# Kernel optimization log

Measured on AMD Instinct MI355X. Metric: run time of the kernel, lower is better.

## Reference

```python
import jax, jax.numpy as jnp
import numpy as np

T, H, E, F, K, FS = 2048, 2048, 64, 512, 8, 512


def setup_inputs() -> dict:
    key = jax.random.key(0)
    ks = jax.random.split(key, 6)
    s = 0.02
    return {
        "hidden_states": jax.random.normal(ks[0], (T, H), jnp.float32),
        # merged gate: E router logits + 1 shared-expert gate logit
        "W_gate": jax.random.normal(ks[1], (H, E + 1), jnp.float32) * s,
        # per-expert merged gate_up proj: [E, H, 2F]
        "W_gate_up": jax.random.normal(ks[2], (E, H, 2 * F), jnp.float32) * s,
        "W_down": jax.random.normal(ks[3], (E, F, H), jnp.float32) * s,
        # shared expert
        "Ws_gate_up": jax.random.normal(ks[4], (H, 2 * FS), jnp.float32) * s,
        "Ws_down": jax.random.normal(ks[5], (FS, H), jnp.float32) * s,
    }


def reference(hidden_states, W_gate, W_gate_up, W_down, Ws_gate_up, Ws_down):
    x = hidden_states  # [T, H]
    logits_all = x @ W_gate                      # [T, E+1]
    router_logits = logits_all[:, :E]
    shared_gate_logit = logits_all[:, E:]        # [T, 1]

    # FusedMoE routing: softmax -> top_k -> renormalize (norm_topk_prob=True)
    probs = jax.nn.softmax(router_logits.astype(jnp.float32), axis=-1)
    topk_w, topk_idx = jax.lax.top_k(probs, K)   # [T, K]
    topk_w = topk_w / jnp.sum(topk_w, axis=-1, keepdims=True)
    # dense combine weights [T, E] (zero for unselected experts)
    combine = jnp.zeros((T, E), probs.dtype).at[
        jnp.arange(T)[:, None], topk_idx].set(topk_w)

    # grouped expert GEMMs (dense reference: every expert sees all tokens,
    # combine-weights zero-out unrouted pairs)
    gu = jnp.einsum('th,ehf->etf', x, W_gate_up)   # [E, T, 2F]
    g, u = jnp.split(gu, 2, axis=-1)
    act = jax.nn.silu(g) * u                       # [E, T, F]
    # apply combine weight before down-proj to avoid [E, T, H] intermediate
    act = act * combine.T[:, :, None].astype(act.dtype)
    routed = jnp.einsum('etf,efh->th', act, W_down)  # [T, H]

    # shared expert (Qwen3NextMLP with sigmoid expert_gate)
    sgu = x @ Ws_gate_up                           # [T, 2FS]
    sg, su = jnp.split(sgu, 2, axis=-1)
    shared = (jax.nn.silu(sg) * su) @ Ws_down      # [T, H]
    shared = jax.nn.sigmoid(shared_gate_logit) * shared

    return shared + routed.astype(x.dtype)
```

## Files before the change

### kernel.cpp

```cpp
#include <hip/hip_runtime.h>
#include <hip/hip_bf16.h>
#include <math.h>

#define T_TOK 2048
#define H_DIM 2048
#define E_NUM 64
#define F_DIM 512
#define K_TOP 8
#define FS_DIM 512
#define NROWS (T_TOK * K_TOP)

typedef __attribute__((ext_vector_type(8))) short short8v;
typedef __attribute__((ext_vector_type(4))) float f32x4;

static __device__ __forceinline__ unsigned short f2bf(float f) {
    unsigned int u = __float_as_uint(f);
    u += 0x7fff + ((u >> 16) & 1);
    return (unsigned short)(u >> 16);
}

#define ASWZ(row) (((row) + ((row) >> 3)) & 7)

typedef const unsigned int __attribute__((address_space(1))) gu32;
typedef unsigned int __attribute__((address_space(3))) lu32;
#define GLDS16(gsrc, ldst) \
    __builtin_amdgcn_global_load_lds((gu32*)(gsrc), (lu32*)(ldst), 16, 0, 0)
#define SB0() __builtin_amdgcn_sched_barrier(0)

__global__ __launch_bounds__(256) void cvt_bf16_kernel(
    const float* __restrict__ in, unsigned short* __restrict__ out, int n8)
{
    int i = blockIdx.x * 256 + threadIdx.x;
    if (i < n8) {
        const float4* p = (const float4*)(in + (size_t)i * 8);
        float4 v0 = p[0], v1 = p[1];
        ushort4 a = make_ushort4(f2bf(v0.x), f2bf(v0.y), f2bf(v0.z), f2bf(v0.w));
        ushort4 b = make_ushort4(f2bf(v1.x), f2bf(v1.y), f2bf(v1.z), f2bf(v1.w));
        ushort4* q = (ushort4*)(out + (size_t)i * 8);
        q[0] = a; q[1] = b;
    }
}

__global__ __launch_bounds__(64) void router_kernel(
    const float* __restrict__ x, const float* __restrict__ Wg,
    int* __restrict__ topk_idx, float* __restrict__ topk_w,
    float* __restrict__ sgate, int* __restrict__ counts)
{
    const int t = blockIdx.x;
    const int lane = threadIdx.x;
    const float* xr = x + (size_t)t * H_DIM;

    float a0 = 0.f, a1 = 0.f, a2 = 0.f, a3 = 0.f;
    for (int h = 0; h < H_DIM; h += 4) {
        float4 xv = *(const float4*)&xr[h];
        a0 += xv.x * Wg[(h + 0) * 65 + lane];
        a1 += xv.y * Wg[(h + 1) * 65 + lane];
        a2 += xv.z * Wg[(h + 2) * 65 + lane];
        a3 += xv.w * Wg[(h + 3) * 65 + lane];
    }
    float logit = (a0 + a1) + (a2 + a3);

    float a64 = 0.f;
    for (int h = lane; h < H_DIM; h += 64) a64 += xr[h] * Wg[h * 65 + 64];
#pragma unroll
    for (int off = 32; off >= 1; off >>= 1) a64 += __shfl_xor(a64, off);

    float v = logit;
    float selv[K_TOP]; int seli[K_TOP];
#pragma unroll
    for (int k = 0; k < K_TOP; ++k) {
        float mv = v; int mi = lane;
#pragma unroll
        for (int off = 32; off >= 1; off >>= 1) {
            float ov = __shfl_xor(mv, off);
            int   oi = __shfl_xor(mi, off);
            if (ov > mv || (ov == mv && oi < mi)) { mv = ov; mi = oi; }
        }
        selv[k] = mv; seli[k] = mi;
        if (lane == mi) v = -INFINITY;
    }

    if (lane == 0) {
        float m = selv[0];
        float w[K_TOP]; float s = 0.f;
#pragma unroll
        for (int k = 0; k < K_TOP; ++k) { w[k] = __expf(selv[k] - m); s += w[k]; }
        float inv = 1.f / s;
#pragma unroll
        for (int k = 0; k < K_TOP; ++k) {
            topk_idx[t * K_TOP + k] = seli[k];
            topk_w[t * K_TOP + k] = w[k] * inv;
            atomicAdd(&counts[seli[k]], 1);
        }
        sgate[t] = 1.f / (1.f + __expf(-a64));
    }
}

__global__ __launch_bounds__(256) void bucket_kernel(
    const int* __restrict__ topk_idx, const float* __restrict__ topk_w,
    const int* __restrict__ counts, int* __restrict__ offsets,
    int* __restrict__ bucket_tok, float* __restrict__ bucket_w)
{
    const int e = blockIdx.x, thr = threadIdx.x;
    __shared__ int cnt[256];
    __shared__ int base_s;
    const int q0 = thr * 64;
    int c = 0;
    for (int q = 0; q < 64; ++q) c += (topk_idx[q0 + q] == e) ? 1 : 0;
    cnt[thr] = c;
    __syncthreads();
    if (thr == 0) {
        int off = 0;
        for (int i = 0; i < e; ++i) off += counts[i];
        offsets[e] = off;
        base_s = off;
        int run = 0;
        for (int i = 0; i < 256; ++i) { int tval = cnt[i]; cnt[i] = run; run += tval; }
    }
    __syncthreads();
    int pos = base_s + cnt[thr];
    for (int q = 0; q < 64; ++q) {
        int pp = q0 + q;
        if (topk_idx[pp] == e) {
            bucket_tok[pos] = pp >> 3;
            bucket_w[pos] = topk_w[pp];
            ++pos;
        }
    }
}

__global__ __launch_bounds__(256) void transpose_cvt_kernel(
    const float* __restrict__ in, unsigned short* __restrict__ out,
    int R, int C)
{
    const int e = blockIdx.z;
    in  += (size_t)e * R * C;
    out += (size_t)e * R * C;
    const int c0 = blockIdx.x * 64, r0 = blockIdx.y * 64;
    __shared__ unsigned short tile[64][72];
    const int t = threadIdx.x;
    const int cc = (t & 15) * 4;
#pragma unroll
    for (int i = 0; i < 4; ++i) {
        int r = (t >> 4) + i * 16;
        float4 v = *(const float4*)&in[(size_t)(r0 + r) * C + c0 + cc];
        tile[cc + 0][r] = f2bf(v.x);
        tile[cc + 1][r] = f2bf(v.y);
        tile[cc + 2][r] = f2bf(v.z);
        tile[cc + 3][r] = f2bf(v.w);
    }
    __syncthreads();
    const int c = t >> 2, j = t & 3;
    uint4 v0 = *(const uint4*)&tile[c][j * 16];
    uint4 v1 = *(const uint4*)&tile[c][j * 16 + 8];
    uint4* dst = (uint4*)&out[(size_t)(c0 + c) * R + r0 + j * 16];
    dst[0] = v0; dst[1] = v1;
}

template<bool ROUTED>
__global__ __launch_bounds__(256, 2) void gu_mfma_kernel(
    const unsigned short* __restrict__ xb,
    const unsigned short* __restrict__ WT,
    const int* __restrict__ counts, const int* __restrict__ offsets,
    const int* __restrict__ bucket_tok, const float* __restrict__ bucket_w,
    unsigned short* __restrict__ actout)
{
    constexpr int BM = 128;
    __shared__ __align__(16) unsigned short As[2][BM * 64];
    __shared__ __align__(16) unsigned short Bs[2][128 * 64];
    __shared__ int   toksS[BM];
    __shared__ float twsS[BM];

    const int tid  = threadIdx.x;
    const int lane = tid & 63;
    const int wid  = tid >> 6;
    const int wm = wid >> 1, wn = wid & 1;
    const int lrow = lane & 15, lhi = lane >> 4;

    int cblk, ne, base, e;
    if (ROUTED) {
        int nw = (blockIdx.x & 7) * ((int)gridDim.x >> 3) + (blockIdx.x >> 3);
        e = nw >> 3; cblk = nw & 7;
        ne = counts[e]; base = offsets[e];
    } else {
        e = E_NUM; cblk = blockIdx.x;
        ne = T_TOK; base = 0;
    }
    const int c0 = cblk * 64;
    const unsigned short* We = WT + (size_t)e * (2 * F_DIM) * H_DIM;

    int rdB[4][2];
#pragma unroll
    for (int fn = 0; fn < 4; ++fn) {
        int r = ((fn & 1) ? 16 : 0) + wn * 32 + lrow + ((fn >> 1) ? 64 : 0);
#pragma unroll
        for (int ks = 0; ks < 2; ++ks) {
            int kc = ks * 4 + lhi;
            rdB[fn][ks] = r * 64 + ((kc ^ ASWZ(r)) & 7) * 8;
        }
    }
    int rdA[4][2];
#pragma unroll
    for (int fm = 0; fm < 4; ++fm) {
        int arow = wm * 64 + fm * 16 + lrow;
#pragma unroll
        for (int ks = 0; ks < 2; ++ks) {
            int kc = ks * 4 + lhi;
            rdA[fm][ks] = arow * 64 + ((kc ^ ASWZ(arow)) & 7) * 8;
        }
    }
    int bsrc[4];
#pragma unroll
    for (int i = 0; i < 4; ++i) {
        int n = wid * 32 + i * 8 + (lane >> 3);
        int grow = (n < 64) ? (c0 + n) : (F_DIM + c0 + (n - 64));
        bsrc[i] = grow * H_DIM + (((lane & 7) ^ ASWZ(n)) << 3);
    }
    const int NT = H_DIM / 64;

    const int m0_beg = ROUTED ? 0 : blockIdx.y * BM;
    const int m0_end = ROUTED ? ne : m0_beg + BM;

    for (int m0 = m0_beg; m0 < m0_end; m0 += BM) {
        __syncthreads();
        if (tid < BM) {
            int idx = m0 + tid; bool v = idx < ne;
            if (ROUTED) {
                toksS[tid] = v ? bucket_tok[base + idx] : bucket_tok[base];
                twsS[tid]  = v ? bucket_w[base + idx] : 0.f;
            } else {
                toksS[tid] = v ? idx : (T_TOK - 1);
                twsS[tid]  = 1.f;
            }
        }
        __syncthreads();

        int asrc[4];
#pragma unroll
        for (int i = 0; i < 4; ++i) {
            int row = wid * 32 + i * 8 + (lane >> 3);
            asrc[i] = toksS[row] * H_DIM + (((lane & 7) ^ ASWZ(row)) << 3);
        }

        f32x4 acc[4][4];
#pragma unroll
        for (int i = 0; i < 4; ++i)
#pragma unroll
            for (int j = 0; j < 4; ++j) acc[i][j] = (f32x4){0.f, 0.f, 0.f, 0.f};

#pragma unroll
        for (int i = 0; i < 4; ++i) GLDS16(xb + asrc[i], &As[0][(wid * 32 + i * 8) * 64]);
#pragma unroll
        for (int i = 0; i < 4; ++i) GLDS16(We + bsrc[i], &Bs[0][(wid * 32 + i * 8) * 64]);
#pragma unroll
        for (int i = 0; i < 4; ++i) GLDS16(xb + asrc[i] + 64, &As[1][(wid * 32 + i * 8) * 64]);
#pragma unroll
        for (int i = 0; i < 4; ++i) GLDS16(We + bsrc[i] + 64, &Bs[1][(wid * 32 + i * 8) * 64]);
        SB0();

        for (int kt = 0; kt < NT; ++kt) {
            if (kt + 1 < NT) asm volatile("s_waitcnt vmcnt(8)" ::: "memory");
            else             asm volatile("s_waitcnt vmcnt(0)" ::: "memory");
            SB0();
            __builtin_amdgcn_s_barrier();
            SB0();
            const unsigned short* A_ = As[kt & 1];
            const unsigned short* B_ = Bs[kt & 1];
            __builtin_amdgcn_s_setprio(1);
#pragma unroll
            for (int ks = 0; ks < 2; ++ks) {
                short8v bf[4];
#pragma unroll
                for (int fn = 0; fn < 4; ++fn) bf[fn] = *(const short8v*)&B_[rdB[fn][ks]];
#pragma unroll
                for (int fm = 0; fm < 4; ++fm) {
                    short8v af = *(const short8v*)&A_[rdA[fm][ks]];
#pragma unroll
                    for (int fn = 0; fn < 4; ++fn)
                        acc[fm][fn] = __builtin_amdgcn_mfma_f32_16x16x32_bf16(
                            af, bf[fn], acc[fm][fn], 0, 0, 0);
                }
            }
            __builtin_amdgcn_s_setprio(0);
            SB0();
            __builtin_amdgcn_s_barrier();
            SB0();
            if (kt + 2 < NT) {
                const int kn = (kt + 2) * 64;
#pragma unroll
                for (int i = 0; i < 4; ++i)
                    GLDS16(xb + asrc[i] + kn, &As[kt & 1][(wid * 32 + i * 8) * 64]);
#pragma unroll
                for (int i = 0; i < 4; ++i)
                    GLDS16(We + bsrc[i] + kn, &Bs[kt & 1][(wid * 32 + i * 8) * 64]);
                SB0();
            }
        }

#pragma unroll
        for (int fm = 0; fm < 4; ++fm) {
#pragma unroll
            for (int p = 0; p < 2; ++p) {
                const int acol = c0 + wn * 32 + p * 16 + lrow;
#pragma unroll
                for (int i = 0; i < 4; ++i) {
                    int ml = wm * 64 + fm * 16 + lhi * 4 + i;
                    int idx = m0 + ml;
                    if (idx < ne) {
                        float gv = acc[fm][p][i], uv = acc[fm][p + 2][i];
                        float sg = gv / (1.f + __expf(-gv));
                        float val = sg * uv * twsS[ml];
                        size_t orow = ROUTED ? (size_t)(base + idx) : (size_t)idx;
                        actout[orow * F_DIM + acol] = f2bf(val);
                    }
                }
            }
        }
    }
}

template<bool ROUTED>
__global__ __launch_bounds__(256, 2) void down_mfma_kernel(
    const unsigned short* __restrict__ actb,
    const unsigned short* __restrict__ WT,
    const int* __restrict__ counts, const int* __restrict__ offsets,
    const int* __restrict__ bucket_tok, const float* __restrict__ sgate,
    float* __restrict__ out)
{
    constexpr int BM = 128;
    __shared__ __align__(16) unsigned short As[2][BM * 64];
    __shared__ __align__(16) unsigned short Bs[2][128 * 64];
    __shared__ int   toksS[BM];
    __shared__ float sgS[BM];

    const int tid  = threadIdx.x;
    const int lane = tid & 63;
    const int wid  = tid >> 6;
    const int wm = wid >> 1, wn = wid & 1;
    const int lrow = lane & 15, lhi = lane >> 4;

    int cblk, ne, base, e;
    if (ROUTED) {
        int nw = (blockIdx.x & 7) * ((int)gridDim.x >> 3) + (blockIdx.x >> 3);
        e = nw >> 4; cblk = nw & 15;
        ne = counts[e]; base = offsets[e];
    } else {
        e = E_NUM; cblk = blockIdx.x;
        ne = T_TOK; base = 0;
    }
    const int c0 = cblk * 128;
    const unsigned short* We = WT + (size_t)e * H_DIM * F_DIM;

    int rdB[4][2];
#pragma unroll
    for (int fn = 0; fn < 4; ++fn) {
        int r = wn * 64 + fn * 16 + lrow;
#pragma unroll
        for (int ks = 0; ks < 2; ++ks) {
            int kc = ks * 4 + lhi;
            rdB[fn][ks] = r * 64 + ((kc ^ ASWZ(r)) & 7) * 8;
        }
    }
    int rdA[4][2];
#pragma unroll
    for (int fm = 0; fm < 4; ++fm) {
        int arow = wm * 64 + fm * 16 + lrow;
#pragma unroll
        for (int ks = 0; ks < 2; ++ks) {
            int kc = ks * 4 + lhi;
            rdA[fm][ks] = arow * 64 + ((kc ^ ASWZ(arow)) & 7) * 8;
        }
    }
    int bsrc[4];
#pragma unroll
    for (int i = 0; i < 4; ++i) {
        int n = wid * 32 + i * 8 + (lane >> 3);
        bsrc[i] = (c0 + n) * F_DIM + (((lane & 7) ^ ASWZ(n)) << 3);
    }
    const int NT = F_DIM / 64;

    const int m0_beg = ROUTED ? 0 : blockIdx.y * BM;
    const int m0_end = ROUTED ? ne : m0_beg + BM;

    for (int m0 = m0_beg; m0 < m0_end; m0 += BM) {
        __syncthreads();
        if (tid < BM) {
            int idx = m0 + tid;
            if (ROUTED) {
                toksS[tid] = (idx < ne) ? bucket_tok[base + idx] : 0;
            } else {
                sgS[tid] = sgate[(idx < ne) ? idx : (T_TOK - 1)];
            }
        }
        __syncthreads();

        int asrc[4];
#pragma unroll
        for (int i = 0; i < 4; ++i) {
            int row = wid * 32 + i * 8 + (lane >> 3);
            int grow = ROUTED ? min(base + m0 + row, NROWS - 1)
                              : min(m0 + row, T_TOK - 1);
            asrc[i] = grow * F_DIM + (((lane & 7) ^ ASWZ(row)) << 3);
        }

        f32x4 acc[4][4];
#pragma unroll
        for (int i = 0; i < 4; ++i)
#pragma unroll
            for (int j = 0; j < 4; ++j) acc[i][j] = (f32x4){0.f, 0.f, 0.f, 0.f};

#pragma unroll
        for (int i = 0; i < 4; ++i) GLDS16(actb + asrc[i], &As[0][(wid * 32 + i * 8) * 64]);
#pragma unroll
        for (int i = 0; i < 4; ++i) GLDS16(We + bsrc[i], &Bs[0][(wid * 32 + i * 8) * 64]);
#pragma unroll
        for (int i = 0; i < 4; ++i) GLDS16(actb + asrc[i] + 64, &As[1][(wid * 32 + i * 8) * 64]);
#pragma unroll
        for (int i = 0; i < 4; ++i) GLDS16(We + bsrc[i] + 64, &Bs[1][(wid * 32 + i * 8) * 64]);
        SB0();

        for (int kt = 0; kt < NT; ++kt) {
            if (kt + 1 < NT) asm volatile("s_waitcnt vmcnt(8)" ::: "memory");
            else             asm volatile("s_waitcnt vmcnt(0)" ::: "memory");
            SB0();
            __builtin_amdgcn_s_barrier();
            SB0();
            const unsigned short* A_ = As[kt & 1];
            const unsigned short* B_ = Bs[kt & 1];
            __builtin_amdgcn_s_setprio(1);
#pragma unroll
            for (int ks = 0; ks < 2; ++ks) {
                short8v bf[4];
#pragma unroll
                for (int fn = 0; fn < 4; ++fn) bf[fn] = *(const short8v*)&B_[rdB[fn][ks]];
#pragma unroll
                for (int fm = 0; fm < 4; ++fm) {
                    short8v af = *(const short8v*)&A_[rdA[fm][ks]];
#pragma unroll
                    for (int fn = 0; fn < 4; ++fn)
                        acc[fm][fn] = __builtin_amdgcn_mfma_f32_16x16x32_bf16(
                            af, bf[fn], acc[fm][fn], 0, 0, 0);
                }
            }
            __builtin_amdgcn_s_setprio(0);
            SB0();
            __builtin_amdgcn_s_barrier();
            SB0();
            if (kt + 2 < NT) {
                const int kn = (kt + 2) * 64;
#pragma unroll
                for (int i = 0; i < 4; ++i)
                    GLDS16(actb + asrc[i] + kn, &As[kt & 1][(wid * 32 + i * 8) * 64]);
#pragma unroll
                for (int i = 0; i < 4; ++i)
                    GLDS16(We + bsrc[i] + kn, &Bs[kt & 1][(wid * 32 + i * 8) * 64]);
                SB0();
            }
        }

#pragma unroll
        for (int fm = 0; fm < 4; ++fm) {
#pragma unroll
            for (int fn = 0; fn < 4; ++fn) {
                int col = c0 + wn * 64 + fn * 16 + lrow;
#pragma unroll
                for (int i = 0; i < 4; ++i) {
                    int ml = wm * 64 + fm * 16 + lhi * 4 + i;
                    int idx = m0 + ml;
                    if (idx < ne) {
                        if (ROUTED)
                            atomicAdd(&out[(size_t)toksS[ml] * H_DIM + col], acc[fm][fn][i]);
                        else
                            out[(size_t)idx * H_DIM + col] = sgS[ml] * acc[fm][fn][i];
                    }
                }
            }
        }
    }
}

extern "C" void kernel_launch(void* const* d_in, const int* in_sizes, int n_in,
                              void* d_out, int out_size, void* d_ws, size_t ws_size,
                              hipStream_t stream) {
    const float* x    = (const float*)d_in[0];
    const float* Wg   = (const float*)d_in[1];
    const float* Wgu  = (const float*)d_in[2];
    const float* Wd   = (const float*)d_in[3];
    const float* Wsgu = (const float*)d_in[4];
    const float* Wsd  = (const float*)d_in[5];
    float* out = (float*)d_out;

    char* p = (char*)d_ws;
    auto alloc = [&](size_t bytes) {
        char* r = p;
        p += (bytes + 255) & ~(size_t)255;
        return r;
    };
    int*   topk_idx   = (int*)  alloc((size_t)T_TOK * K_TOP * sizeof(int));
    float* topk_w     = (float*)alloc((size_t)T_TOK * K_TOP * sizeof(float));
    float* sgate      = (float*)alloc((size_t)T_TOK * sizeof(float));
    int*   counts     = (int*)  alloc((size_t)E_NUM * sizeof(int));
    int*   offsets    = (int*)  alloc((size_t)E_NUM * sizeof(int));
    int*   bucket_tok = (int*)  alloc((size_t)NROWS * sizeof(int));
    float* bucket_w   = (float*)alloc((size_t)NROWS * sizeof(float));
    unsigned short* xb    = (unsigned short*)alloc((size_t)T_TOK * H_DIM * 2);
    unsigned short* act_r = (unsigned short*)alloc((size_t)NROWS * F_DIM * 2);
    unsigned short* act_s = (unsigned short*)alloc((size_t)T_TOK * FS_DIM * 2);
    unsigned short* WTgu = (unsigned short*)alloc((size_t)65 * (2 * F_DIM) * H_DIM * 2);
    unsigned short* WTd  = (unsigned short*)alloc((size_t)65 * H_DIM * F_DIM * 2);

    hipMemsetAsync(counts, 0, E_NUM * sizeof(int), stream);
    cvt_bf16_kernel<<<(T_TOK * H_DIM / 8 + 255) / 256, 256, 0, stream>>>(x, xb, T_TOK * H_DIM / 8);
    router_kernel<<<T_TOK, 64, 0, stream>>>(x, Wg, topk_idx, topk_w, sgate, counts);
    bucket_kernel<<<E_NUM, 256, 0, stream>>>(topk_idx, topk_w, counts, offsets, bucket_tok, bucket_w);

    transpose_cvt_kernel<<<dim3((2 * F_DIM) / 64, H_DIM / 64, E_NUM), 256, 0, stream>>>(
        Wgu, WTgu, H_DIM, 2 * F_DIM);
    transpose_cvt_kernel<<<dim3((2 * FS_DIM) / 64, H_DIM / 64, 1), 256, 0, stream>>>(
        Wsgu, WTgu + (size_t)64 * (2 * F_DIM) * H_DIM, H_DIM, 2 * FS_DIM);
    transpose_cvt_kernel<<<dim3(H_DIM / 64, F_DIM / 64, E_NUM), 256, 0, stream>>>(
        Wd, WTd, F_DIM, H_DIM);
    transpose_cvt_kernel<<<dim3(H_DIM / 64, FS_DIM / 64, 1), 256, 0, stream>>>(
        Wsd, WTd + (size_t)64 * H_DIM * F_DIM, FS_DIM, H_DIM);

    gu_mfma_kernel<true><<<8 * E_NUM, 256, 0, stream>>>(
        xb, WTgu, counts, offsets, bucket_tok, bucket_w, act_r);
    gu_mfma_kernel<false><<<dim3(8, T_TOK / 128), 256, 0, stream>>>(
        xb, WTgu, counts, offsets, bucket_tok, bucket_w, act_s);

    down_mfma_kernel<false><<<dim3(16, T_TOK / 128), 256, 0, stream>>>(
        act_s, WTd, counts, offsets, bucket_tok, sgate, out);
    down_mfma_kernel<true><<<16 * E_NUM, 256, 0, stream>>>(
        act_r, WTd, counts, offsets, bucket_tok, sgate, out);
}
```

Before: 792.7 us.

## Use K=32 triple-buffered LDS tiles, raise occupancy, split routed gate-up M-tiles

Both MFMA GEMM kernels now stage 32-wide K tiles in a three-deep LDS ring instead of 64-wide tiles double-buffered, with a matching 4-chunk XOR swizzle and half as many global-to-LDS loads per step. The smaller LDS footprint lets launch bounds request three blocks per CU, aiming to hide memory latency through occupancy. The routed gate-up kernel splits each expert's token range across two interleaved M-tile blocks (1024 blocks, empty ones exit early) to spread uneven expert loads more evenly. In exchange there are twice as many barrier-separated K iterations, each doing less MFMA work, which adds sync overhead.

Measured after the change: 847.3 us. 6.9% more time.

```diff
diff --git a/kernel.cpp b/kernel.cpp
--- a/kernel.cpp
+++ b/kernel.cpp
@@ -19,7 +19,7 @@
     return (unsigned short)(u >> 16);
 }
 
-#define ASWZ(row) (((row) + ((row) >> 3)) & 7)
+#define ASW32(r) (((r) >> 1) & 3)
 
 typedef const unsigned int __attribute__((address_space(1))) gu32;
 typedef unsigned int __attribute__((address_space(3))) lu32;
@@ -158,7 +158,7 @@
 }
 
 template<bool ROUTED>
-__global__ __launch_bounds__(256, 2) void gu_mfma_kernel(
+__global__ __launch_bounds__(256, 3) void gu_mfma_kernel(
     const unsigned short* __restrict__ xb,
     const unsigned short* __restrict__ WT,
     const int* __restrict__ counts, const int* __restrict__ offsets,
@@ -166,8 +166,8 @@
     unsigned short* __restrict__ actout)
 {
     constexpr int BM = 128;
-    __shared__ __align__(16) unsigned short As[2][BM * 64];
-    __shared__ __align__(16) unsigned short Bs[2][128 * 64];
+    __shared__ __align__(16) unsigned short As[3][BM * 32];
+    __shared__ __align__(16) unsigned short Bs[3][128 * 32];
     __shared__ int   toksS[BM];
     __shared__ float twsS[BM];
 
@@ -177,51 +177,46 @@
     const int wm = wid >> 1, wn = wid & 1;
     const int lrow = lane & 15, lhi = lane >> 4;
 
-    int cblk, ne, base, e;
+    int cblk, ne, base, e, m0_beg, m0_end, m0_stride;
     if (ROUTED) {
-        int nw = (blockIdx.x & 7) * ((int)gridDim.x >> 3) + (blockIdx.x >> 3);
-        e = nw >> 3; cblk = nw & 7;
+        int nw = (blockIdx.x & 7) * 128 + (blockIdx.x >> 3);
+        e = nw >> 4;
+        int mt = (nw >> 3) & 1;
+        cblk = nw & 7;
         ne = counts[e]; base = offsets[e];
+        if (mt * BM >= ne) return;
+        m0_beg = mt * BM; m0_end = ne; m0_stride = 2 * BM;
     } else {
         e = E_NUM; cblk = blockIdx.x;
         ne = T_TOK; base = 0;
+        m0_beg = blockIdx.y * BM; m0_end = m0_beg + BM; m0_stride = BM;
     }
     const int c0 = cblk * 64;
     const unsigned short* We = WT + (size_t)e * (2 * F_DIM) * H_DIM;
 
-    int rdB[4][2];
+    int rdB[4];
 #pragma unroll
     for (int fn = 0; fn < 4; ++fn) {
         int r = ((fn & 1) ? 16 : 0) + wn * 32 + lrow + ((fn >> 1) ? 64 : 0);
-#pragma unroll
-        for (int ks = 0; ks < 2; ++ks) {
-            int kc = ks * 4 + lhi;
-            rdB[fn][ks] = r * 64 + ((kc ^ ASWZ(r)) & 7) * 8;
-        }
-    }
-    int rdA[4][2];
+        rdB[fn] = r * 32 + ((lhi ^ ASW32(r)) << 3);
+    }
+    int rdA[4];
 #pragma unroll
     for (int fm = 0; fm < 4; ++fm) {
         int arow = wm * 64 + fm * 16 + lrow;
-#pragma unroll
-        for (int ks = 0; ks < 2; ++ks) {
-            int kc = ks * 4 + lhi;
-            rdA[fm][ks] = arow * 64 + ((kc ^ ASWZ(arow)) & 7) * 8;
-        }
-    }
-    int bsrc[4];
-#pragma unroll
-    for (int i = 0; i < 4; ++i) {
-        int n = wid * 32 + i * 8 + (lane >> 3);
+        rdA[fm] = arow * 32 + ((lhi ^ ASW32(arow)) << 3);
+    }
+    int bsrc[2], brow[2];
+#pragma unroll
+    for (int i = 0; i < 2; ++i) {
+        int n = wid * 32 + i * 16 + (lane >> 2);
         int grow = (n < 64) ? (c0 + n) : (F_DIM + c0 + (n - 64));
-        bsrc[i] = grow * H_DIM + (((lane & 7) ^ ASWZ(n)) << 3);
-    }
-    const int NT = H_DIM / 64;
-
-    const int m0_beg = ROUTED ? 0 : blockIdx.y * BM;
-    const int m0_end = ROUTED ? ne : m0_beg + BM;
-
-    for (int m0 = m0_beg; m0 < m0_end; m0 += BM) {
+        brow[i] = n;
+        bsrc[i] = grow * H_DIM + (((lane & 3) ^ ASW32(n)) << 3);
+    }
+    const int NT = H_DIM / 32;
+
+    for (int m0 = m0_beg; m0 < m0_end; m0 += m0_stride) {
         __syncthreads();
         if (tid < BM) {
             int idx = m0 + tid; bool v = idx < ne;
@@ -235,11 +230,11 @@
         }
         __syncthreads();
 
-        int asrc[4];
-#pragma unroll
-        for (int i = 0; i < 4; ++i) {
-            int row = wid * 32 + i * 8 + (lane >> 3);
-            asrc[i] = toksS[row] * H_DIM + (((lane & 7) ^ ASWZ(row)) << 3);
+        int asrc[2];
+#pragma unroll
+        for (int i = 0; i < 2; ++i) {
+            int row = wid * 32 + i * 16 + (lane >> 2);
+            asrc[i] = toksS[row] * H_DIM + (((lane & 3) ^ ASW32(row)) << 3);
         }
 
         f32x4 acc[4][4];
@@ -249,50 +244,51 @@
             for (int j = 0; j < 4; ++j) acc[i][j] = (f32x4){0.f, 0.f, 0.f, 0.f};
 
 #pragma unroll
-        for (int i = 0; i < 4; ++i) GLDS16(xb + asrc[i], &As[0][(wid * 32 + i * 8) * 64]);
-#pragma unroll
-        for (int i = 0; i < 4; ++i) GLDS16(We + bsrc[i], &Bs[0][(wid * 32 + i * 8) * 64]);
-#pragma unroll
-        for (int i = 0; i < 4; ++i) GLDS16(xb + asrc[i] + 64, &As[1][(wid * 32 + i * 8) * 64]);
-#pragma unroll
-        for (int i = 0; i < 4; ++i) GLDS16(We + bsrc[i] + 64, &Bs[1][(wid * 32 + i * 8) * 64]);
+        for (int tt = 0; tt < 2; ++tt) {
+            const int k0 = tt * 32;
+#pragma unroll
+            for (int i = 0; i < 2; ++i)
+                GLDS16(xb + asrc[i] + k0, &As[tt][(wid * 32 + i * 16) * 32]);
+#pragma unroll
+            for (int i = 0; i < 2; ++i)
+                GLDS16(We + bsrc[i] + k0, &Bs[tt][(wid * 32 + i * 16) * 32]);
+        }
         SB0();
 
         for (int kt = 0; kt < NT; ++kt) {
-            if (kt + 1 < NT) asm volatile("s_waitcnt vmcnt(8)" ::: "memory");
+            if (kt + 1 < NT) asm volatile("s_waitcnt vmcnt(4)" ::: "memory");
             else             asm volatile("s_waitcnt vmcnt(0)" ::: "memory");
             SB0();
             __builtin_amdgcn_s_barrier();
             SB0();
-            const unsigned short* A_ = As[kt & 1];
-            const unsigned short* B_ = Bs[kt & 1];
+            const unsigned short* A_ = As[kt % 3];
+            const unsigned short* B_ = Bs[kt % 3];
             __builtin_amdgcn_s_setprio(1);
-#pragma unroll
-            for (int ks = 0; ks < 2; ++ks) {
-                short8v bf[4];
-#pragma unroll
-                for (int fn = 0; fn < 4; ++fn) bf[fn] = *(const short8v*)&B_[rdB[fn][ks]];
-#pragma unroll
-                for (int fm = 0; fm < 4; ++fm) {
-                    short8v af = *(const short8v*)&A_[rdA[fm][ks]];
-#pragma unroll
-                    for (int fn = 0; fn < 4; ++fn)
-                        acc[fm][fn] = __builtin_amdgcn_mfma_f32_16x16x32_bf16(
-                            af, bf[fn], acc[fm][fn], 0, 0, 0);
-                }
+            short8v bf[4];
+#pragma unroll
+            for (int fn = 0; fn < 4; ++fn) bf[fn] = *(const short8v*)&B_[rdB[fn]];
+#pragma unroll
+            for (int fm = 0; fm < 4; ++fm) {
+                short8v af = *(const short8v*)&A_[rdA[fm]];
+#pragma unroll
+                for (int fn = 0; fn < 4; ++fn)
+                    acc[fm][fn] = __builtin_amdgcn_mfma_f32_16x16x32_bf16(
+                        af, bf[fn], acc[fm][fn], 0, 0, 0);
             }
             __builtin_amdgcn_s_setprio(0);
             SB0();
             __builtin_amdgcn_s_barrier();
             SB0();
             if (kt + 2 < NT) {
-                const int kn = (kt + 2) * 64;
-#pragma unroll
-                for (int i = 0; i < 4; ++i)
-                    GLDS16(xb + asrc[i] + kn, &As[kt & 1][(wid * 32 + i * 8) * 64]);
-#pragma unroll
-                for (int i = 0; i < 4; ++i)
-                    GLDS16(We + bsrc[i] + kn, &Bs[kt & 1][(wid * 32 + i * 8) * 64]);
+                const int kn = (kt + 2) * 32;
+                unsigned short* An = As[(kt + 2) % 3];
+                unsigned short* Bn = Bs[(kt + 2) % 3];
+#pragma unroll
+                for (int i = 0; i < 2; ++i)
+                    GLDS16(xb + asrc[i] + kn, &An[(wid * 32 + i * 16) * 32]);
+#pragma unroll
+                for (int i = 0; i < 2; ++i)
+                    GLDS16(We + bsrc[i] + kn, &Bn[(wid * 32 + i * 16) * 32]);
                 SB0();
             }
         }
@@ -320,7 +316,7 @@
 }
 
 template<bool ROUTED>
-__global__ __launch_bounds__(256, 2) void down_mfma_kernel(
+__global__ __launch_bounds__(256, 3) void down_mfma_kernel(
     const unsigned short* __restrict__ actb,
     const unsigned short* __restrict__ WT,
     const int* __restrict__ counts, const int* __restrict__ offsets,
@@ -328,8 +324,8 @@
     float* __restrict__ out)
 {
     constexpr int BM = 128;
-    __shared__ __align__(16) unsigned short As[2][BM * 64];
-    __shared__ __align__(16) unsigned short Bs[2][128 * 64];
+    __shared__ __align__(16) unsigned short As[3][BM * 32];
+    __shared__ __align__(16) unsigned short Bs[3][128 * 32];
     __shared__ int   toksS[BM];
     __shared__ float sgS[BM];
 
@@ -341,7 +337,7 @@
 
     int cblk, ne, base, e;
     if (ROUTED) {
-        int nw = (blockIdx.x & 7) * ((int)gridDim.x >> 3) + (blockIdx.x >> 3);
+        int nw = (blockIdx.x & 7) * 128 + (blockIdx.x >> 3);
         e = nw >> 4; cblk = nw & 15;
         ne = counts[e]; base = offsets[e];
     } else {
@@ -351,33 +347,25 @@
     const int c0 = cblk * 128;
     const unsigned short* We = WT + (size_t)e * H_DIM * F_DIM;
 
-    int rdB[4][2];
+    int rdB[4];
 #pragma unroll
     for (int fn = 0; fn < 4; ++fn) {
         int r = wn * 64 + fn * 16 + lrow;
-#pragma unroll
-        for (int ks = 0; ks < 2; ++ks) {
-            int kc = ks * 4 + lhi;
-            rdB[fn][ks] = r * 64 + ((kc ^ ASWZ(r)) & 7) * 8;
-        }
-    }
-    int rdA[4][2];
+        rdB[fn] = r * 32 + ((lhi ^ ASW32(r)) << 3);
+    }
+    int rdA[4];
 #pragma unroll
     for (int fm = 0; fm < 4; ++fm) {
         int arow = wm * 64 + fm * 16 + lrow;
-#pragma unroll
-        for (int ks = 0; ks < 2; ++ks) {
-            int kc = ks * 4 + lhi;
-            rdA[fm][ks] = arow * 64 + ((kc ^ ASWZ(arow)) & 7) * 8;
-        }
-    }
-    int bsrc[4];
-#pragma unroll
-    for (int i = 0; i < 4; ++i) {
-        int n = wid * 32 + i * 8 + (lane >> 3);
-        bsrc[i] = (c0 + n) * F_DIM + (((lane & 7) ^ ASWZ(n)) << 3);
-    }
-    const int NT = F_DIM / 64;
+        rdA[fm] = arow * 32 + ((lhi ^ ASW32(arow)) << 3);
+    }
+    int bsrc[2];
+#pragma unroll
+    for (int i = 0; i < 2; ++i) {
+        int n = wid * 32 + i * 16 + (lane >> 2);
+        bsrc[i] = (c0 + n) * F_DIM + (((lane & 3) ^ ASW32(n)) << 3);
+    }
+    const int NT = F_DIM / 32;
 
     const int m0_beg = ROUTED ? 0 : blockIdx.y * BM;
     const int m0_end = ROUTED ? ne : m0_beg + BM;
@@ -394,13 +382,13 @@
         }
         __syncthreads();
 
-        int asrc[4];
-#pragma unroll
-        for (int i = 0; i < 4; ++i) {
-            int row = wid * 32 + i * 8 + (lane >> 3);
+        int asrc[2];
+#pragma unroll
+        for (int i = 0; i < 2; ++i) {
+            int row = wid * 32 + i * 16 + (lane >> 2);
             int grow = ROUTED ? min(base + m0 + row, NROWS - 1)
                               : min(m0 + row, T_TOK - 1);
-            asrc[i] = grow * F_DIM + (((lane & 7) ^ ASWZ(row)) << 3);
+            asrc[i] = grow * F_DIM + (((lane & 3) ^ ASW32(row)) << 3);
         }
 
         f32x4 acc[4][4];
@@ -410,50 +398,51 @@
             for (int j = 0; j < 4; ++j) acc[i][j] = (f32x4){0.f, 0.f, 0.f, 0.f};
 
 #pragma unroll
-        for (int i = 0; i < 4; ++i) GLDS16(actb + asrc[i], &As[0][(wid * 32 + i * 8) * 64]);
-#pragma unroll
-        for (int i = 0; i < 4; ++i) GLDS16(We + bsrc[i], &Bs[0][(wid * 32 + i * 8) * 64]);
-#pragma unroll
-        for (int i = 0; i < 4; ++i) GLDS16(actb + asrc[i] + 64, &As[1][(wid * 32 + i * 8) * 64]);
-#pragma unroll
-        for (int i = 0; i < 4; ++i) GLDS16(We + bsrc[i] + 64, &Bs[1][(wid * 32 + i * 8) * 64]);
+        for (int tt = 0; tt < 2; ++tt) {
+            const int k0 = tt * 32;
+#pragma unroll
+            for (int i = 0; i < 2; ++i)
+                GLDS16(actb + asrc[i] + k0, &As[tt][(wid * 32 + i * 16) * 32]);
+#pragma unroll
+            for (int i = 0; i < 2; ++i)
+                GLDS16(We + bsrc[i] + k0, &Bs[tt][(wid * 32 + i * 16) * 32]);
+        }
         SB0();
 
         for (int kt = 0; kt < NT; ++kt) {
-            if (kt + 1 < NT) asm volatile("s_waitcnt vmcnt(8)" ::: "memory");
+            if (kt + 1 < NT) asm volatile("s_waitcnt vmcnt(4)" ::: "memory");
             else             asm volatile("s_waitcnt vmcnt(0)" ::: "memory");
             SB0();
             __builtin_amdgcn_s_barrier();
             SB0();
-            const unsigned short* A_ = As[kt & 1];
-            const unsigned short* B_ = Bs[kt & 1];
+            const unsigned short* A_ = As[kt % 3];
+            const unsigned short* B_ = Bs[kt % 3];
             __builtin_amdgcn_s_setprio(1);
-#pragma unroll
-            for (int ks = 0; ks < 2; ++ks) {
-                short8v bf[4];
-#pragma unroll
-                for (int fn = 0; fn < 4; ++fn) bf[fn] = *(const short8v*)&B_[rdB[fn][ks]];
-#pragma unroll
-                for (int fm = 0; fm < 4; ++fm) {
-                    short8v af = *(const short8v*)&A_[rdA[fm][ks]];
-#pragma unroll
-                    for (int fn = 0; fn < 4; ++fn)
-                        acc[fm][fn] = __builtin_amdgcn_mfma_f32_16x16x32_bf16(
-                            af, bf[fn], acc[fm][fn], 0, 0, 0);
-                }
+            short8v bf[4];
+#pragma unroll
+            for (int fn = 0; fn < 4; ++fn) bf[fn] = *(const short8v*)&B_[rdB[fn]];
+#pragma unroll
+            for (int fm = 0; fm < 4; ++fm) {
+                short8v af = *(const short8v*)&A_[rdA[fm]];
+#pragma unroll
+                for (int fn = 0; fn < 4; ++fn)
+                    acc[fm][fn] = __builtin_amdgcn_mfma_f32_16x16x32_bf16(
+                        af, bf[fn], acc[fm][fn], 0, 0, 0);
             }
             __builtin_amdgcn_s_setprio(0);
             SB0();
             __builtin_amdgcn_s_barrier();
             SB0();
             if (kt + 2 < NT) {
-                const int kn = (kt + 2) * 64;
-#pragma unroll
-                for (int i = 0; i < 4; ++i)
-                    GLDS16(actb + asrc[i] + kn, &As[kt & 1][(wid * 32 + i * 8) * 64]);
-#pragma unroll
-                for (int i = 0; i < 4; ++i)
-                    GLDS16(We + bsrc[i] + kn, &Bs[kt & 1][(wid * 32 + i * 8) * 64]);
+                const int kn = (kt + 2) * 32;
+                unsigned short* An = As[(kt + 2) % 3];
+                unsigned short* Bn = Bs[(kt + 2) % 3];
+#pragma unroll
+                for (int i = 0; i < 2; ++i)
+                    GLDS16(actb + asrc[i] + kn, &An[(wid * 32 + i * 16) * 32]);
+#pragma unroll
+                for (int i = 0; i < 2; ++i)
+                    GLDS16(We + bsrc[i] + kn, &Bn[(wid * 32 + i * 16) * 32]);
                 SB0();
             }
         }
@@ -523,13 +512,13 @@
     transpose_cvt_kernel<<<dim3(H_DIM / 64, FS_DIM / 64, 1), 256, 0, stream>>>(
         Wsd, WTd + (size_t)64 * H_DIM * F_DIM, FS_DIM, H_DIM);
 
-    gu_mfma_kernel<true><<<8 * E_NUM, 256, 0, stream>>>(
+    gu_mfma_kernel<true><<<1024, 256, 0, stream>>>(
         xb, WTgu, counts, offsets, bucket_tok, bucket_w, act_r);
     gu_mfma_kernel<false><<<dim3(8, T_TOK / 128), 256, 0, stream>>>(
         xb, WTgu, counts, offsets, bucket_tok, bucket_w, act_s);
 
     down_mfma_kernel<false><<<dim3(16, T_TOK / 128), 256, 0, stream>>>(
         act_s, WTd, counts, offsets, bucket_tok, sgate, out);
-    down_mfma_kernel<true><<<16 * E_NUM, 256, 0, stream>>>(
+    down_mfma_kernel<true><<<1024, 256, 0, stream>>>(
         act_r, WTd, counts, offsets, bucket_tok, sgate, out);
 }
```
